# Kernel tuning notes

Hardware: AMD Instinct MI355X
Metric: run time of the kernel (lower is better)

Reference implementation:

```python
import jax, jax.numpy as jnp
import numpy as np

B, L, N = 32, 64, 8
C, H_IMG, W_IMG = 3, 40, 40
HID = 64
N_ACT = 8
CNN_OUT = 64  # 64 channels * 1 * 1 spatial after the three convs on 40x40


def _conv(x, w, b, stride):
    # x: (B', Cin, H, W), w: (Cout, Cin, kh, kw)
    y = jax.lax.conv_general_dilated(
        x, w, window_strides=(stride, stride), padding='VALID',
        dimension_numbers=('NCHW', 'OIHW', 'NCHW'))
    return y + b[None, :, None, None]


def setup_inputs() -> dict:
    key = jax.random.key(0)
    ks = jax.random.split(key, 12)

    def rn(k, shape, fan_in):
        return jax.random.normal(k, shape, dtype=jnp.float32) * (1.0 / np.sqrt(fan_in))

    inp = {
        'obs_batch': jax.random.normal(ks[0], (B, L, N, C, H_IMG, W_IMG), dtype=jnp.float32),
        'hidden_state': jnp.zeros((B, N, HID), dtype=jnp.float32),
        'conv1_w': rn(ks[1], (32, C, 8, 8), C * 8 * 8),
        'conv1_b': jnp.zeros((32,), jnp.float32),
        'conv2_w': rn(ks[2], (64, 32, 4, 4), 32 * 4 * 4),
        'conv2_b': jnp.zeros((64,), jnp.float32),
        'conv3_w': rn(ks[3], (64, 64, 3, 3), 64 * 3 * 3),
        'conv3_b': jnp.zeros((64,), jnp.float32),
        'w_ih': rn(ks[4], (3 * HID, CNN_OUT), CNN_OUT),
        'w_hh': rn(ks[5], (3 * HID, HID), HID),
        'b_ih': jnp.zeros((3 * HID,), jnp.float32),
        'b_hh': jnp.zeros((3 * HID,), jnp.float32),
        'fc_w': rn(ks[6], (N_ACT, HID), HID),
        'fc_b': jnp.zeros((N_ACT,), jnp.float32),
    }
    return inp


def reference(obs_batch, hidden_state, conv1_w, conv1_b, conv2_w, conv2_b,
              conv3_w, conv3_b, w_ih, w_hh, b_ih, b_hh, fc_w, fc_b):
    b, l, n = obs_batch.shape[:3]
    x = obs_batch.reshape(-1, C, H_IMG, W_IMG)            # (B*L*N, C, H, W)
    x = jax.nn.relu(_conv(x, conv1_w, conv1_b, 4))
    x = jax.nn.relu(_conv(x, conv2_w, conv2_b, 2))
    x = jax.nn.relu(_conv(x, conv3_w, conv3_b, 1))
    feats = x.reshape(b, l, n, -1)                        # (B, L, N, F)

    # (L, B*N, F) time-major for scan
    rnn_in = feats.transpose(1, 0, 2, 3).reshape(l, b * n, -1)
    h0 = hidden_state.reshape(b * n, HID)

    def step(h, xt):
        gi = xt @ w_ih.T + b_ih
        gh = h @ w_hh.T + b_hh
        i_r, i_z, i_n = jnp.split(gi, 3, axis=-1)
        h_r, h_z, h_n = jnp.split(gh, 3, axis=-1)
        r = jax.nn.sigmoid(i_r + h_r)
        z = jax.nn.sigmoid(i_z + h_z)
        nn_ = jnp.tanh(i_n + r * h_n)
        h_new = (1.0 - z) * nn_ + z * h
        return h_new, h_new

    h_last, hs = jax.lax.scan(step, h0, rnn_in)           # hs: (L, B*N, HID)

    # torch path: stack (L, B*N, H) -> permute to (B*N, L, H) -> reshape (B*L*N, H)
    rnn_out = hs.transpose(1, 0, 2).reshape(b, n, l, HID).transpose(0, 2, 1, 3)
    q = rnn_out.reshape(-1, HID) @ fc_w.T + fc_b
    q_values = q.reshape(b, l, n, N_ACT)
    next_hidden_state = h_last.reshape(b, n, HID)
    return q_values, next_hidden_state
```

## Files before the change

kernel.cpp:

```cpp
#include <hip/hip_runtime.h>
#include <math.h>

typedef unsigned short ushort_t;
typedef unsigned int uint_t;
typedef __attribute__((ext_vector_type(8))) short short8_t;
typedef __attribute__((ext_vector_type(4))) float f32x4_t;

constexpr int Bb = 32, Ll = 64, Nn = 8;
constexpr int IMGS = Bb * Ll * Nn;
constexpr int Cc = 3, Hh = 40, Ww = 40;
constexpr int HID = 64, G3 = 192, NACT = 8;

__device__ inline float bf2f(ushort_t u) {
  union { uint_t i; float f; } v; v.i = ((uint_t)u) << 16; return v.f;
}
__device__ inline ushort_t f2bf(float f) {
  union { float f; uint_t u; } v; v.f = f;
  uint_t r = v.u + 0x7fffu + ((v.u >> 16) & 1u);
  return (ushort_t)(r >> 16);
}
__device__ inline void unpack2(uint_t u, float& lo, float& hi) {
  union { uint_t i; float f; } a, b;
  a.i = u << 16; b.i = u & 0xffff0000u;
  lo = a.f; hi = b.f;
}
__device__ inline float ld1(const void* p, int idx, int isbf) {
  return isbf ? bf2f(((const ushort_t*)p)[idx]) : ((const float*)p)[idx];
}
__device__ inline short8_t ldsh8(const ushort_t* p) {
  union { short8_t v; uint2 u[2]; } r;
  r.u[0] = *(const uint2*)p;
  r.u[1] = *(const uint2*)(p + 4);
  return r.v;
}
__device__ inline short8_t ldg8(const ushort_t* p) {
  union { short8_t v; uint4 u; } r;
  r.u = *(const uint4*)p;
  return r.v;
}
#define WAVE_FENCE() asm volatile("s_waitcnt lgkmcnt(0)" ::: "memory")

__global__ __launch_bounds__(256) void detect_kernel(
    const ushort_t* __restrict__ obs, const ushort_t* __restrict__ whh,
    int* __restrict__ flags) {
  __shared__ int cnt[2];
  if (threadIdx.x < 2) cnt[threadIdx.x] = 0;
  __syncthreads();
  int bad0 = 0, bad1 = 0;
  for (int i = threadIdx.x; i < 4096; i += 256) {
    int e0 = (obs[i] >> 7) & 0xFF; if (e0 >= 0xC0) bad0++;
    int e1 = (whh[i] >> 7) & 0xFF; if (e1 >= 0xC0) bad1++;
  }
  atomicAdd(&cnt[0], bad0);
  atomicAdd(&cnt[1], bad1);
  __syncthreads();
  if (threadIdx.x == 0) { flags[0] = (cnt[0] <= 4); flags[1] = (cnt[1] <= 4); }
}

__global__ __launch_bounds__(256) void repack_kernel(
    const void* __restrict__ w1, const void* __restrict__ w2,
    const void* __restrict__ w3, const void* __restrict__ wih,
    const int* __restrict__ flags,
    ushort_t* __restrict__ w1pack, ushort_t* __restrict__ w2pack,
    ushort_t* __restrict__ w3bf, ushort_t* __restrict__ wihb) {
  const int fw = flags[1];
  int t = blockIdx.x * 256 + threadIdx.x;
  if (t < 6144) w1pack[t] = f2bf(ld1(w1, t, fw));
  if (t < 32768) {
    int oc = t >> 9, r = t & 511;
    int kykx = r >> 5, ic = r & 31;
    w2pack[t] = f2bf(ld1(w2, oc * 512 + ic * 16 + kykx, fw));
  }
  if (t < 36864) w3bf[t] = f2bf(ld1(w3, t, fw));
  if (t < 12288) wihb[t] = f2bf(ld1(wih, t, fw));
}

__global__ __launch_bounds__(256) void conv12_kernel(
    const void* __restrict__ obs, const ushort_t* __restrict__ w1pack,
    const ushort_t* __restrict__ w2pack,
    const void* __restrict__ b1, const void* __restrict__ b2,
    const int* __restrict__ flags, ushort_t* __restrict__ f2g, int img_base) {
  __shared__ __attribute__((aligned(16))) ushort_t s_mem[4][4800];

  const int tid = threadIdx.x;
  const int wave = tid >> 6, lane = tid & 63;
  const int lrow = lane & 15, lk8 = lane >> 4;
  const int fobs = flags[0], fw = flags[1];
  const int img0 = blockIdx.x * 4;

  if (fobs) {
    const uint4* src = reinterpret_cast<const uint4*>((const ushort_t*)obs + ((size_t)img_base + img0) * 4800);
    for (int i = tid; i < 2400; i += 256) {
      const int im_ = i / 600, e = i - im_ * 600;
      reinterpret_cast<uint4*>(s_mem[im_])[e] = src[im_ * 600 + e];
    }
  } else {
    const float4* src = reinterpret_cast<const float4*>((const float*)obs + ((size_t)img_base + img0) * 4800);
    for (int i = tid; i < 4800; i += 256) {
      const int im_ = i / 1200, e = i - im_ * 1200;
      float4 v = src[im_ * 1200 + e];
      uint2 o;
      o.x = (uint_t)f2bf(v.x) | ((uint_t)f2bf(v.y) << 16);
      o.y = (uint_t)f2bf(v.z) | ((uint_t)f2bf(v.w) << 16);
      reinterpret_cast<uint2*>(s_mem[im_])[e] = o;
    }
  }
  __syncthreads();

  {
    ushort_t* si = s_mem[wave];
    int ab[6];
#pragma unroll
    for (int mt = 0; mt < 6; ++mt) {
      int p = mt * 16 + lrow; if (p > 80) p = 80;
      ab[mt] = (p / 9) * 160 + (p % 9) * 4;
    }
    f32x4_t acc[2][6];
#pragma unroll
    for (int nt = 0; nt < 2; ++nt)
#pragma unroll
      for (int mt = 0; mt < 6; ++mt) acc[nt][mt] = (f32x4_t){0.f, 0.f, 0.f, 0.f};
    const ushort_t* wr0 = w1pack + lrow * 192 + lk8 * 8;
#pragma unroll
    for (int ks = 0; ks < 6; ++ks) {
      const int g = ks * 4 + lk8;
      const int aoff = (g >> 3) * 1600 + (g & 7) * 40;
      short8_t b0 = ldg8(wr0 + ks * 32);
      short8_t b1v = ldg8(wr0 + 16 * 192 + ks * 32);
#pragma unroll
      for (int mt = 0; mt < 6; ++mt) {
        short8_t a = ldsh8(&si[aoff + ab[mt]]);
        acc[0][mt] = __builtin_amdgcn_mfma_f32_16x16x32_bf16(a, b0, acc[0][mt], 0, 0, 0);
        acc[1][mt] = __builtin_amdgcn_mfma_f32_16x16x32_bf16(a, b1v, acc[1][mt], 0, 0, 0);
      }
    }
    WAVE_FENCE();
    const float bz0 = ld1(b1, lrow, fw), bz1 = ld1(b1, 16 + lrow, fw);
#pragma unroll
    for (int mt = 0; mt < 6; ++mt) {
#pragma unroll
      for (int r = 0; r < 4; ++r) {
        const int p = mt * 16 + lk8 * 4 + r;
        if (p < 81) {
          si[p * 40 + lrow]      = f2bf(fmaxf(acc[0][mt][r] + bz0, 0.f));
          si[p * 40 + 16 + lrow] = f2bf(fmaxf(acc[1][mt][r] + bz1, 0.f));
        }
      }
    }
  }
  __syncthreads();

  {
    int imgr[3], pbx[3];
#pragma unroll
    for (int mt = 0; mt < 3; ++mt) {
      int row = mt * 16 + lrow; if (row > 35) row = 35;
      const int ir = row / 9, p2 = row - ir * 9;
      imgr[mt] = ir;
      pbx[mt] = (p2 / 3) * 18 + (p2 % 3) * 2;
    }
    f32x4_t acc[3];
#pragma unroll
    for (int mt = 0; mt < 3; ++mt) acc[mt] = (f32x4_t){0.f, 0.f, 0.f, 0.f};
    const ushort_t* w2r = w2pack + (wave * 16 + lrow) * 512 + lk8 * 8;
#pragma unroll
    for (int s = 0; s < 16; ++s) {
      const int po = (s >> 2) * 9 + (s & 3);
      short8_t bv = ldg8(w2r + s * 32);
      short8_t a0 = ldsh8(&s_mem[imgr[0]][(pbx[0] + po) * 40 + lk8 * 8]);
      short8_t a1 = ldsh8(&s_mem[imgr[1]][(pbx[1] + po) * 40 + lk8 * 8]);
      short8_t a2 = ldsh8(&s_mem[imgr[2]][(pbx[2] + po) * 40 + lk8 * 8]);
      acc[0] = __builtin_amdgcn_mfma_f32_16x16x32_bf16(a0, bv, acc[0], 0, 0, 0);
      acc[1] = __builtin_amdgcn_mfma_f32_16x16x32_bf16(a1, bv, acc[1], 0, 0, 0);
      acc[2] = __builtin_amdgcn_mfma_f32_16x16x32_bf16(a2, bv, acc[2], 0, 0, 0);
    }
    const int oc = wave * 16 + lrow;
    const float bias = ld1(b2, oc, fw);
#pragma unroll
    for (int mt = 0; mt < 3; ++mt) {
#pragma unroll
      for (int r = 0; r < 4; ++r) {
        const int row = mt * 16 + lk8 * 4 + r;
        if (row < 36) {
          const int ir = row / 9, pp = row - ir * 9;
          f2g[((size_t)img_base + img0 + ir) * 576 + oc * 9 + pp] =
              f2bf(fmaxf(acc[mt][r] + bias, 0.f));
        }
      }
    }
  }
}

__global__ __launch_bounds__(256) void conv3gi_kernel(
    const ushort_t* __restrict__ f2g, const ushort_t* __restrict__ w3bf,
    const ushort_t* __restrict__ wihb, const void* __restrict__ b3,
    const int* __restrict__ flags, float* __restrict__ gi, int img_base) {
  __shared__ __attribute__((aligned(16))) ushort_t f2b[16 * 592];
  __shared__ __attribute__((aligned(16))) ushort_t f3b[16 * 72];

  const int tid = threadIdx.x;
  const int wave = tid >> 6, lane = tid & 63;
  const int lrow = lane & 15, lk8 = lane >> 4;
  const int fw = flags[1];
  const int iloc0 = blockIdx.x * 16;

  for (int i = tid; i < 16 * 72; i += 256) {
    const int im_ = i / 72, off = i - im_ * 72;
    *reinterpret_cast<uint4*>(&f2b[im_ * 592 + off * 8]) =
        *reinterpret_cast<const uint4*>(&f2g[((size_t)img_base + iloc0 + im_) * 576 + off * 8]);
  }
  __syncthreads();

  {
    f32x4_t c3 = (f32x4_t){0.f, 0.f, 0.f, 0.f};
    const ushort_t* w3r = w3bf + (wave * 16 + lrow) * 576 + lk8 * 8;
#pragma unroll
    for (int ks = 0; ks < 18; ++ks) {
      short8_t a = ldsh8(&f2b[lrow * 592 + ks * 32 + lk8 * 8]);
      short8_t bv = ldg8(w3r + ks * 32);
      c3 = __builtin_amdgcn_mfma_f32_16x16x32_bf16(a, bv, c3, 0, 0, 0);
    }
    const int oc = wave * 16 + lrow;
    const float bias = ld1(b3, oc, fw);
#pragma unroll
    for (int r = 0; r < 4; ++r)
      f3b[(lk8 * 4 + r) * 72 + oc] = f2bf(fmaxf(c3[r] + bias, 0.f));
  }
  __syncthreads();

#pragma unroll
  for (int t = 0; t < 3; ++t) {
    const int nt = wave * 3 + t;
    f32x4_t g = (f32x4_t){0.f, 0.f, 0.f, 0.f};
#pragma unroll
    for (int ks = 0; ks < 2; ++ks) {
      short8_t a = ldsh8(&f3b[lrow * 72 + ks * 32 + lk8 * 8]);
      short8_t bv = ldg8(wihb + (nt * 16 + lrow) * 64 + ks * 32 + lk8 * 8);
      g = __builtin_amdgcn_mfma_f32_16x16x32_bf16(a, bv, g, 0, 0, 0);
    }
#pragma unroll
    for (int r = 0; r < 4; ++r)
      gi[((size_t)img_base + iloc0 + lk8 * 4 + r) * G3 + nt * 16 + lrow] = g[r];
  }
}

__global__ __launch_bounds__(64) void gru_kernel(
    const float* __restrict__ gi, const void* __restrict__ h0,
    const void* __restrict__ whh, const void* __restrict__ bih,
    const void* __restrict__ bhh, const int* __restrict__ flags,
    float* __restrict__ rnn, float* __restrict__ hout) {
  __shared__ float s_w[G3 * 68];
  __shared__ float s_h[HID];
  const int j = threadIdx.x;
  const int s = blockIdx.x;
  const int fw = flags[1];

  if (fw) {
    const uint4* wsrc = reinterpret_cast<const uint4*>(whh);
    for (int v = j; v < (G3 * HID) / 8; v += 64) {
      uint4 w = wsrc[v];
      int i8 = v * 8;
      float* d = &s_w[(i8 >> 6) * 68 + (i8 & 63)];
      unpack2(w.x, d[0], d[1]);
      unpack2(w.y, d[2], d[3]);
      unpack2(w.z, d[4], d[5]);
      unpack2(w.w, d[6], d[7]);
    }
  } else {
    const float4* wsrc = reinterpret_cast<const float4*>(whh);
    for (int v = j; v < (G3 * HID) / 4; v += 64) {
      float4 w = wsrc[v];
      int i4 = v * 4;
      float* d = &s_w[(i4 >> 6) * 68 + (i4 & 63)];
      d[0] = w.x; d[1] = w.y; d[2] = w.z; d[3] = w.w;
    }
  }
  float h = ld1(h0, s * HID + j, fw);
  s_h[j] = h;
  const float bir = ld1(bih, j, fw), biz = ld1(bih, 64 + j, fw), bin_ = ld1(bih, 128 + j, fw);
  const float bhr = ld1(bhh, j, fw), bhz = ld1(bhh, 64 + j, fw), bhn = ld1(bhh, 128 + j, fw);
  const int b = s >> 3, n = s & 7;
  const float* gbase = gi + ((size_t)b * Ll * Nn + n) * G3;
  float* rbase = rnn + ((size_t)b * Ll * Nn + n) * HID;
  __syncthreads();

  const float* wr = &s_w[j * 68];
  const float* wz = &s_w[(64 + j) * 68];
  const float* wn = &s_w[(128 + j) * 68];

  float g0 = gbase[j], g1 = gbase[64 + j], g2 = gbase[128 + j];

  for (int l = 0; l < Ll; ++l) {
    float p0 = 0.f, p1 = 0.f, p2 = 0.f;
    if (l + 1 < Ll) {
      const float* gn = gbase + (size_t)(l + 1) * Nn * G3;
      p0 = gn[j]; p1 = gn[64 + j]; p2 = gn[128 + j];
    }
    float hr = bhr, hz = bhz, hn = bhn;
#pragma unroll 4
    for (int k = 0; k < 64; k += 4) {
      float4 hv = *reinterpret_cast<const float4*>(&s_h[k]);
      float4 w0 = *reinterpret_cast<const float4*>(wr + k);
      float4 w1v = *reinterpret_cast<const float4*>(wz + k);
      float4 w2v = *reinterpret_cast<const float4*>(wn + k);
      hr += w0.x * hv.x + w0.y * hv.y + w0.z * hv.z + w0.w * hv.w;
      hz += w1v.x * hv.x + w1v.y * hv.y + w1v.z * hv.z + w1v.w * hv.w;
      hn += w2v.x * hv.x + w2v.y * hv.y + w2v.z * hv.z + w2v.w * hv.w;
    }
    const float gr = g0 + bir + hr;
    const float gz = g1 + biz + hz;
    const float gn_ = g2 + bin_;
    const float r = 1.f / (1.f + __expf(-gr));
    const float z = 1.f / (1.f + __expf(-gz));
    const float nn_ = tanhf(gn_ + r * hn);
    h = (1.f - z) * nn_ + z * h;
    __syncthreads();
    s_h[j] = h;
    rbase[(size_t)l * Nn * HID + j] = h;
    __syncthreads();
    g0 = p0; g1 = p1; g2 = p2;
  }
  hout[(size_t)s * HID + j] = h;
}

__global__ __launch_bounds__(256) void fc_kernel(
    const float* __restrict__ rnn, const void* __restrict__ fcw,
    const void* __restrict__ fcb, const int* __restrict__ flags,
    float* __restrict__ q) {
  __shared__ float s_w[NACT * HID];
  __shared__ float s_b[NACT];
  const int tid = threadIdx.x;
  const int fw = flags[1];
  for (int i = tid; i < NACT * HID; i += 256) s_w[i] = ld1(fcw, i, fw);
  if (tid < NACT) s_b[tid] = ld1(fcb, tid, fw);
  __syncthreads();
  const int row = blockIdx.x * 256 + tid;
  float x[64];
  const float4* xp = reinterpret_cast<const float4*>(rnn + (size_t)row * HID);
#pragma unroll
  for (int i = 0; i < 16; ++i) {
    float4 v = xp[i];
    x[4 * i] = v.x; x[4 * i + 1] = v.y; x[4 * i + 2] = v.z; x[4 * i + 3] = v.w;
  }
#pragma unroll
  for (int a = 0; a < NACT; ++a) {
    float v = s_b[a];
#pragma unroll
    for (int k = 0; k < 64; ++k) v += x[k] * s_w[a * 64 + k];
    q[(size_t)row * NACT + a] = v;
  }
}

extern "C" void kernel_launch(void* const* d_in, const int* in_sizes, int n_in,
                              void* d_out, int out_size, void* d_ws, size_t ws_size,
                              hipStream_t stream) {
  const void* obs = d_in[0];
  const void* h0  = d_in[1];
  const void* w1  = d_in[2];
  const void* b1  = d_in[3];
  const void* w2  = d_in[4];
  const void* b2  = d_in[5];
  const void* w3  = d_in[6];
  const void* b3  = d_in[7];
  const void* wih = d_in[8];
  const void* whh = d_in[9];
  const void* bih = d_in[10];
  const void* bhh = d_in[11];
  const void* fcw = d_in[12];
  const void* fcb = d_in[13];

  float* qout = (float*)d_out;
  float* hout = qout + (size_t)IMGS * NACT;

  char* wsb = (char*)d_ws;
  int*      flags  = (int*)wsb;
  float*    gi     = (float*)(wsb + 16);
  float*    rnn    = gi + (size_t)IMGS * G3;
  ushort_t* w1pack = (ushort_t*)(rnn + (size_t)IMGS * HID);
  ushort_t* w2pack = w1pack + 6144;
  ushort_t* w3bf   = w2pack + 32768;
  ushort_t* wihb   = w3bf + 36864;
  ushort_t* f2g    = wihb + 12288;

  const size_t base_bytes = (size_t)((char*)f2g - wsb);
  size_t cap = (ws_size > base_bytes) ? (ws_size - base_bytes) / 1152 : 0;
  cap = (cap / 16) * 16;
  if (cap > (size_t)IMGS) cap = IMGS;

  detect_kernel<<<1, 256, 0, stream>>>((const ushort_t*)obs, (const ushort_t*)whh, flags);
  repack_kernel<<<144, 256, 0, stream>>>(w1, w2, w3, wih, flags, w1pack, w2pack, w3bf, wihb);

  for (int c0 = 0; c0 < IMGS; c0 += (int)cap) {
    int n = IMGS - c0; if (n > (int)cap) n = (int)cap;
    conv12_kernel<<<n / 4, 256, 0, stream>>>(obs, w1pack, w2pack, b1, b2, flags, f2g, c0);
    conv3gi_kernel<<<n / 16, 256, 0, stream>>>(f2g, w3bf, wihb, b3, flags, gi, c0);
  }

  gru_kernel<<<256, 64, 0, stream>>>(gi, h0, whh, bih, bhh, flags, rnn, hout);
  fc_kernel<<<IMGS / 256, 256, 0, stream>>>(rnn, fcw, fcb, flags, qout);
}
```

Baseline: 232.4 us.

## Batch global loads in conv12 and GRU setup; use wave fences in GRU loop

The conv12 input staging now issues all global loads into registers before writing to LDS, which raises memory-level parallelism, and the kernel gets an occupancy hint in its launch bounds. The GRU kernel launches 256 threads so the recurrent weight matrix is loaded cooperatively, then exits three waves so the recurrence runs in one wave. Inside the recurrence, block barriers are replaced with a wave-level fence. This relies on WAVE_FENCE being defined in the hidden part of the file, and on a single wave being correct without a full barrier.

```diff
diff --git a/kernel.cpp b/kernel.cpp
--- a/kernel.cpp
+++ b/kernel.cpp
@@ -75,7 +75,7 @@
   if (t < 12288) wihb[t] = f2bf(ld1(wih, t, fw));
 }
 
-__global__ __launch_bounds__(256) void conv12_kernel(
+__global__ __launch_bounds__(256, 4) void conv12_kernel(
     const void* __restrict__ obs, const ushort_t* __restrict__ w1pack,
     const ushort_t* __restrict__ w2pack,
     const void* __restrict__ b1, const void* __restrict__ b2,
@@ -90,19 +90,41 @@
 
   if (fobs) {
     const uint4* src = reinterpret_cast<const uint4*>((const ushort_t*)obs + ((size_t)img_base + img0) * 4800);
-    for (int i = tid; i < 2400; i += 256) {
-      const int im_ = i / 600, e = i - im_ * 600;
-      reinterpret_cast<uint4*>(s_mem[im_])[e] = src[im_ * 600 + e];
+    uint4 r[10];
+#pragma unroll
+    for (int it = 0; it < 10; ++it) {
+      const int i = it * 256 + tid;
+      r[it] = src[i < 2400 ? i : 2399];
+    }
+#pragma unroll
+    for (int it = 0; it < 10; ++it) {
+      const int i = it * 256 + tid;
+      if (i < 2400) {
+        const int im_ = i / 600, e = i - im_ * 600;
+        reinterpret_cast<uint4*>(s_mem[im_])[e] = r[it];
+      }
     }
   } else {
     const float4* src = reinterpret_cast<const float4*>((const float*)obs + ((size_t)img_base + img0) * 4800);
-    for (int i = tid; i < 4800; i += 256) {
-      const int im_ = i / 1200, e = i - im_ * 1200;
-      float4 v = src[im_ * 1200 + e];
-      uint2 o;
-      o.x = (uint_t)f2bf(v.x) | ((uint_t)f2bf(v.y) << 16);
-      o.y = (uint_t)f2bf(v.z) | ((uint_t)f2bf(v.w) << 16);
-      reinterpret_cast<uint2*>(s_mem[im_])[e] = o;
+#pragma unroll
+    for (int bb = 0; bb < 2; ++bb) {
+      float4 r[10];
+#pragma unroll
+      for (int it = 0; it < 10; ++it) {
+        const int i = (bb * 10 + it) * 256 + tid;
+        r[it] = src[i < 4800 ? i : 4799];
+      }
+#pragma unroll
+      for (int it = 0; it < 10; ++it) {
+        const int i = (bb * 10 + it) * 256 + tid;
+        if (i < 4800) {
+          const int im_ = i / 1200, e = i - im_ * 1200;
+          uint2 o;
+          o.x = (uint_t)f2bf(r[it].x) | ((uint_t)f2bf(r[it].y) << 16);
+          o.y = (uint_t)f2bf(r[it].z) | ((uint_t)f2bf(r[it].w) << 16);
+          reinterpret_cast<uint2*>(s_mem[im_])[e] = o;
+        }
+      }
     }
   }
   __syncthreads();
@@ -244,45 +266,59 @@
   }
 }
 
-__global__ __launch_bounds__(64) void gru_kernel(
+__global__ __launch_bounds__(256) void gru_kernel(
     const float* __restrict__ gi, const void* __restrict__ h0,
     const void* __restrict__ whh, const void* __restrict__ bih,
     const void* __restrict__ bhh, const int* __restrict__ flags,
     float* __restrict__ rnn, float* __restrict__ hout) {
   __shared__ float s_w[G3 * 68];
   __shared__ float s_h[HID];
-  const int j = threadIdx.x;
+  const int tid = threadIdx.x;
   const int s = blockIdx.x;
   const int fw = flags[1];
 
   if (fw) {
     const uint4* wsrc = reinterpret_cast<const uint4*>(whh);
-    for (int v = j; v < (G3 * HID) / 8; v += 64) {
-      uint4 w = wsrc[v];
-      int i8 = v * 8;
+    uint4 r[6];
+#pragma unroll
+    for (int it = 0; it < 6; ++it) r[it] = wsrc[it * 256 + tid];
+#pragma unroll
+    for (int it = 0; it < 6; ++it) {
+      const int v = it * 256 + tid;
+      const int i8 = v * 8;
       float* d = &s_w[(i8 >> 6) * 68 + (i8 & 63)];
-      unpack2(w.x, d[0], d[1]);
-      unpack2(w.y, d[2], d[3]);
-      unpack2(w.z, d[4], d[5]);
-      unpack2(w.w, d[6], d[7]);
+      unpack2(r[it].x, d[0], d[1]);
+      unpack2(r[it].y, d[2], d[3]);
+      unpack2(r[it].z, d[4], d[5]);
+      unpack2(r[it].w, d[6], d[7]);
     }
   } else {
     const float4* wsrc = reinterpret_cast<const float4*>(whh);
-    for (int v = j; v < (G3 * HID) / 4; v += 64) {
-      float4 w = wsrc[v];
-      int i4 = v * 4;
-      float* d = &s_w[(i4 >> 6) * 68 + (i4 & 63)];
-      d[0] = w.x; d[1] = w.y; d[2] = w.z; d[3] = w.w;
-    }
-  }
-  float h = ld1(h0, s * HID + j, fw);
-  s_h[j] = h;
+#pragma unroll
+    for (int bb = 0; bb < 2; ++bb) {
+      float4 r[6];
+#pragma unroll
+      for (int it = 0; it < 6; ++it) r[it] = wsrc[(bb * 6 + it) * 256 + tid];
+#pragma unroll
+      for (int it = 0; it < 6; ++it) {
+        const int v = (bb * 6 + it) * 256 + tid;
+        const int i4 = v * 4;
+        float* d = &s_w[(i4 >> 6) * 68 + (i4 & 63)];
+        d[0] = r[it].x; d[1] = r[it].y; d[2] = r[it].z; d[3] = r[it].w;
+      }
+    }
+  }
+  if (tid < 64) s_h[tid] = ld1(h0, s * HID + tid, fw);
+  __syncthreads();
+  if (tid >= 64) return;
+
+  const int j = tid;
+  float h = s_h[j];
   const float bir = ld1(bih, j, fw), biz = ld1(bih, 64 + j, fw), bin_ = ld1(bih, 128 + j, fw);
   const float bhr = ld1(bhh, j, fw), bhz = ld1(bhh, 64 + j, fw), bhn = ld1(bhh, 128 + j, fw);
   const int b = s >> 3, n = s & 7;
   const float* gbase = gi + ((size_t)b * Ll * Nn + n) * G3;
   float* rbase = rnn + ((size_t)b * Ll * Nn + n) * HID;
-  __syncthreads();
 
   const float* wr = &s_w[j * 68];
   const float* wz = &s_w[(64 + j) * 68];
@@ -314,10 +350,10 @@
     const float z = 1.f / (1.f + __expf(-gz));
     const float nn_ = tanhf(gn_ + r * hn);
     h = (1.f - z) * nn_ + z * h;
-    __syncthreads();
+    WAVE_FENCE();
     s_h[j] = h;
     rbase[(size_t)l * Nn * HID + j] = h;
-    __syncthreads();
+    WAVE_FENCE();
     g0 = p0; g1 = p1; g2 = p2;
   }
   hout[(size_t)s * HID + j] = h;
@@ -396,6 +432,6 @@
     conv3gi_kernel<<<n / 16, 256, 0, stream>>>(f2g, w3bf, wihb, b3, flags, gi, c0);
   }
 
-  gru_kernel<<<256, 64, 0, stream>>>(gi, h0, whh, bih, bhh, flags, rnn, hout);
+  gru_kernel<<<256, 256, 0, stream>>>(gi, h0, whh, bih, bhh, flags, rnn, hout);
   fc_kernel<<<IMGS / 256, 256, 0, stream>>>(rnn, fcw, fcb, flags, qout);
 }
```

Result: faster. 216.0 us (-7.1%).
